# Optimization experiments

Measured on AMD Instinct MI355X. Metric: run time of the kernel, lower is better.

The kernel has to match this reference:

```python
import jax, jax.numpy as jnp
import numpy as np

VOC, TOPIC, EMB, BATCH = 128000, 512, 1024, 1024

def setup_inputs() -> dict:
    key = jax.random.key(0)
    k1, k2, k3 = jax.random.split(key, 3)
    x = jax.random.normal(k1, (TOPIC, BATCH), dtype=jnp.float32)
    beta0 = jax.random.normal(k2, (VOC, EMB), dtype=jnp.float32)
    beta_t = jax.random.normal(k3, (TOPIC, EMB), dtype=jnp.float32) * 0.02  # nn.init.normal_(std=0.02)
    return {"x": x, "beta0": beta0, "beta_t": beta_t, "t": 0}

def reference(x, beta0, beta_t, t):
    # w: [voc, topic] = beta0 [voc, emb] @ beta_t.T [emb, topic]
    # (the t==0 branch and else branch are identical in the source)
    w = jnp.einsum('ve,te->vt', beta0, beta_t)
    w = jax.nn.softmax(w, axis=0)  # softmax over vocab dim (dim=0)
    # out: [voc, batch]
    return jnp.einsum('vt,tb->vb', w, x)
```

## Files before the change

kernel.cpp:

```cpp
#include <hip/hip_runtime.h>

typedef _Float16 f16x8 __attribute__((ext_vector_type(8)));
typedef float    f32x4 __attribute__((ext_vector_type(4)));
typedef unsigned short u16;

#define VOC   128000
#define TOPIC 512
#define EMB   1024
#define BATCH 1024
#define ROWB  128

__device__ __forceinline__ int swz(int row, int kbyte) {
    return row * ROWB + (kbyte ^ ((row & 7) << 4));
}
__device__ __forceinline__ int xcd_swz(int bid, int nwg) {
    int x = bid & 7, o = bid >> 3, q = nwg >> 3, r = nwg & 7;
    return (x < r ? x * (q + 1) : r * (q + 1) + (x - r) * q) + o;
}
union H2U { _Float16 h; u16 u; };

#define SBAR() asm volatile("s_barrier" ::: "memory")
#define WVM0() asm volatile("s_waitcnt vmcnt(0)" ::: "memory")
#define WLG0() asm volatile("s_waitcnt lgkmcnt(0)" ::: "memory")

#define GLDS(SRC, DST) __builtin_amdgcn_global_load_lds( \
    (const __attribute__((address_space(1))) unsigned int*)(SRC), \
    (__attribute__((address_space(3))) unsigned int*)(DST), 16, 0, 0)

#define RD_A(MH, KS) { _Pragma("unroll") \
    for (int m = 0; m < 4; ++m) \
        af[m] = *(const f16x8*)(bufA + wr * 16384 + \
            swz((MH) * 64 + m * 16 + lr, (KS) * 64 + lk * 16)); }
#define RD_B(KS) { _Pragma("unroll") \
    for (int n = 0; n < 4; ++n) \
        bf[n] = *(const f16x8*)(bufB + (wc >> 1) * 16384 + \
            swz((wc & 1) * 64 + n * 16 + lr, (KS) * 64 + lk * 16)); }
#define MFMA16(MH) { \
    __builtin_amdgcn_s_setprio(1); \
    _Pragma("unroll") for (int m = 0; m < 4; ++m) \
    _Pragma("unroll") for (int n = 0; n < 4; ++n) \
        acc[(MH) * 4 + m][n] = __builtin_amdgcn_mfma_f32_16x16x32_f16( \
            af[m], bf[n], acc[(MH) * 4 + m][n], 0, 0, 0); \
    __builtin_amdgcn_s_setprio(0); }

__global__ void cvt_betat_kernel(const float* __restrict__ betat, u16* __restrict__ bt16) {
    const size_t g = (size_t)blockIdx.x * 256 + threadIdx.x;
    const float4* src = reinterpret_cast<const float4*>(betat) + g * 2;
    float4 a = src[0], b = src[1];
    f16x8 h;
    h[0]=(_Float16)a.x; h[1]=(_Float16)a.y; h[2]=(_Float16)a.z; h[3]=(_Float16)a.w;
    h[4]=(_Float16)b.x; h[5]=(_Float16)b.y; h[6]=(_Float16)b.z; h[7]=(_Float16)b.w;
    *(reinterpret_cast<f16x8*>(bt16) + g) = h;
}

__global__ __launch_bounds__(512, 2) void gemm1_kernel(
    const float* __restrict__ beta0, const u16* __restrict__ bt16,
    u16* __restrict__ Eg, float* __restrict__ sg)
{
    __shared__ char lds[131072];

    const int tid  = threadIdx.x;
    const int lane = tid & 63;
    const int wid  = tid >> 6;
    const int wr = wid >> 2, wc = wid & 3;
    const int lr = lane & 15, lk = lane >> 4;
    const int srow8  = lane >> 3;
    const int schunk = ((lane & 7) ^ srow8) * 8;

    const int bid   = xcd_swz(blockIdx.x, gridDim.x);
    const int tile  = bid >> 1;
    const int chunk = bid & 1;
    const int v0 = tile * 256, t0 = chunk * 256;

    const int a_row = tid >> 1, a_kh = tid & 1;
    const float* aRowP = beta0 + (size_t)(v0 + a_row) * EMB + a_kh * 32;

    f32x4 acc[8][4] = {};
    f16x8 af[4], bf[4];
    float4 rA[8];

    auto loadA4 = [&](int kt, int j0) {
        const float4* g = reinterpret_cast<const float4*>(aRowP + kt * 64);
        #pragma unroll
        for (int j = 0; j < 4; ++j) rA[j0 + j] = g[j0 + j];
    };
    auto cvtA = [&](int kt1, int j0) {
        char* dA = lds + (kt1 & 1) * 65536 + (a_row >> 7) * 16384;
        const int rl = a_row & 127;
        #pragma unroll
        for (int jj = 0; jj < 2; ++jj) {
            float4 xx = rA[j0 + jj * 2], yy = rA[j0 + jj * 2 + 1];
            f16x8 h;
            h[0]=(_Float16)xx.x; h[1]=(_Float16)xx.y; h[2]=(_Float16)xx.z; h[3]=(_Float16)xx.w;
            h[4]=(_Float16)yy.x; h[5]=(_Float16)yy.y; h[6]=(_Float16)yy.z; h[7]=(_Float16)yy.w;
            *(f16x8*)(dA + swz(rl, (a_kh * 4 + (j0 >> 1) + jj) * 16)) = h;
        }
    };
    auto stageB = [&](int kt, int h) {
        char* dstb = lds + (kt & 1) * 65536 + 32768 + h * 16384;
        #pragma unroll
        for (int q = 0; q < 2; ++q) {
            const u16* s_ = bt16 + (size_t)(t0 + h * 128 + wid * 16 + q * 8 + srow8) * EMB
                          + kt * 64 + schunk;
            GLDS(s_, dstb + (wid * 16 + q * 8) * ROWB);
        }
    };

    loadA4(0, 0); loadA4(0, 4);
    stageB(0, 0); stageB(0, 1);
    cvtA(0, 0); cvtA(0, 4);
    WLG0();

    for (int t = 0; t < 16; ++t) {
        char* bufA = lds + (t & 1) * 65536;
        char* bufB = bufA + 32768;
        const bool st = (t + 1) < 16;

        WVM0();
        SBAR();
        RD_A(0, 0); RD_B(0);
        if (st) { loadA4(t + 1, 0); stageB(t + 1, 0); }
        MFMA16(0);
        SBAR();
        RD_A(1, 0);
        if (st) { loadA4(t + 1, 4); stageB(t + 1, 1); }
        MFMA16(1);
        SBAR();
        RD_A(0, 1); RD_B(1);
        if (st) cvtA(t + 1, 0);
        MFMA16(0);
        SBAR();
        RD_A(1, 1);
        if (st) cvtA(t + 1, 4);
        MFMA16(1);
        WLG0();
    }

    __syncthreads();
    u16* ldsE = reinterpret_cast<u16*>(lds);
    float csum = 0.f;
    #pragma unroll
    for (int c = 0; c < 4; ++c) {
        if (wr == (c >> 1)) {
            const int mb = (c & 1) * 4;
            #pragma unroll
            for (int m = 0; m < 4; ++m)
              #pragma unroll
              for (int n = 0; n < 4; ++n)
                #pragma unroll
                for (int r = 0; r < 4; ++r) {
                    const int row = m * 16 + lk * 4 + r;
                    const int col = wc * 64 + n * 16 + lr;
                    H2U cv; cv.h = (_Float16)__expf(acc[mb + m][n][r]);
                    ldsE[row * 264 + col] = cv.u;
                }
        }
        __syncthreads();
        {
            const int row8 = tid >> 3, seg = tid & 7;
            const int4* sp = reinterpret_cast<const int4*>(&ldsE[row8 * 264 + seg * 32]);
            u16* dst = Eg + (size_t)(v0 + c * 64 + row8) * 2048 + t0 + seg * 32;
            int4 a0 = sp[0], a1 = sp[1], a2 = sp[2], a3 = sp[3];
            int4* dp = reinterpret_cast<int4*>(dst);
            dp[0] = a0; dp[1] = a1; dp[2] = a2; dp[3] = a3;
        }
        if (tid < 256) {
            float s = 0.f;
            for (int r = 0; r < 64; ++r) { H2U cv; cv.u = ldsE[r * 264 + tid]; s += (float)cv.h; }
            csum += s;
        }
        __syncthreads();
    }
    if (tid < 256) atomicAdd(sg + t0 + tid, csum);
}

__global__ void xst_kernel(const float* __restrict__ x, const float* __restrict__ s,
                           u16* __restrict__ xsT)
{
    __shared__ float tile[32][33];
    const int b0 = blockIdx.x * 32, t0 = blockIdx.y * 32;
    const int tx = threadIdx.x, ty = threadIdx.y;
    tile[ty][tx] = x[(size_t)(t0 + ty) * BATCH + b0 + tx];
    __syncthreads();
    const float sc = 65536.0f / s[t0 + tx];
    H2U cv; cv.h = (_Float16)(tile[tx][ty] * sc);
    xsT[(size_t)(b0 + ty) * TOPIC + t0 + tx] = cv.u;
}

__global__ __launch_bounds__(512, 2) void gemm2_kernel(
    const u16* __restrict__ Eg, const u16* __restrict__ xsT,
    float* __restrict__ out, int c0, int nch)
{
    __shared__ char lds[131072];

    const int tid  = threadIdx.x;
    const int lane = tid & 63;
    const int wid  = tid >> 6;
    const int wr = wid >> 2, wc = wid & 3;
    const int lr = lane & 15, lk = lane >> 4;
    const int srow8  = lane >> 3;
    const int schunk = ((lane & 7) ^ srow8) * 8;

    const int bid   = xcd_swz(blockIdx.x, gridDim.x);
    const int tile  = bid / nch;
    const int chunk = bid % nch;
    const int v0 = tile * 256, b0 = (c0 + chunk) * 256;

    f32x4 acc[8][4] = {};
    f16x8 af[4], bf[4];

    auto stageA = [&](int kt, int h) {
        char* dsta = lds + (kt & 1) * 65536 + h * 16384;
        #pragma unroll
        for (int q = 0; q < 2; ++q) {
            const u16* s_ = Eg + (size_t)(v0 + h * 128 + wid * 16 + q * 8 + srow8) * 2048
                          + kt * 64 + schunk;
            GLDS(s_, dsta + (wid * 16 + q * 8) * ROWB);
        }
    };
    auto stageB = [&](int kt, int h) {
        char* dstb = lds + (kt & 1) * 65536 + 32768 + h * 16384;
        #pragma unroll
        for (int q = 0; q < 2; ++q) {
            const u16* s_ = xsT + (size_t)(b0 + h * 128 + wid * 16 + q * 8 + srow8) * TOPIC
                          + kt * 64 + schunk;
            GLDS(s_, dstb + (wid * 16 + q * 8) * ROWB);
        }
    };

    stageA(0, 0); stageA(0, 1); stageB(0, 0); stageB(0, 1);

    for (int t = 0; t < 8; ++t) {
        char* bufA = lds + (t & 1) * 65536;
        char* bufB = bufA + 32768;
        const bool st = (t + 1) < 8;

        WVM0();
        SBAR();
        RD_A(0, 0); RD_B(0);
        if (st) stageA(t + 1, 0);
        MFMA16(0);
        SBAR();
        RD_A(1, 0);
        if (st) stageA(t + 1, 1);
        MFMA16(1);
        SBAR();
        RD_A(0, 1); RD_B(1);
        if (st) stageB(t + 1, 0);
        MFMA16(0);
        SBAR();
        RD_A(1, 1);
        if (st) stageB(t + 1, 1);
        MFMA16(1);
    }

    #pragma unroll
    for (int mh = 0; mh < 2; ++mh)
      #pragma unroll
      for (int m = 0; m < 4; ++m)
        #pragma unroll
        for (int n = 0; n < 4; ++n)
          #pragma unroll
          for (int r = 0; r < 4; ++r) {
              const int row = wr * 128 + mh * 64 + m * 16 + lk * 4 + r;
              const int col = wc * 64 + n * 16 + lr;
              out[(size_t)(v0 + row) * BATCH + b0 + col] = acc[mh * 4 + m][n][r] * 0x1p-16f;
          }
}

extern "C" void kernel_launch(void* const* d_in, const int* in_sizes, int n_in,
                              void* d_out, int out_size, void* d_ws, size_t ws_size,
                              hipStream_t stream)
{
    const float* x     = (const float*)d_in[0];
    const float* beta0 = (const float*)d_in[1];
    const float* betat = (const float*)d_in[2];
    float* out = (float*)d_out;

    const size_t need_min = 4096 + (size_t)BATCH * TOPIC * 2;
    if (ws_size < need_min) return;
    float* s_g  = (float*)d_ws;
    u16*   buf1 = (u16*)((char*)d_ws + 4096);

    hipMemsetAsync(d_ws, 0, 2048, stream);
    cvt_betat_kernel<<<256, 256, 0, stream>>>(betat, buf1);

    u16* EgO = (u16*)d_out;
    gemm1_kernel<<<1000, 512, 0, stream>>>(beta0, buf1, EgO, s_g);

    xst_kernel<<<dim3(BATCH / 32, TOPIC / 32), dim3(32, 32), 0, stream>>>(x, s_g, buf1);

    gemm2_kernel<<<1500, 512, 0, stream>>>(EgO, buf1, out, 1, 3);
    gemm2_kernel<<<500,  512, 0, stream>>>(EgO, buf1, out, 0, 1);
}
```

Measured before the change: 569.5 us.

## Replace pipelined 256x256 GEMM kernels with simple single-buffered 128-tile versions

Both GEMM kernels drop the double-buffered, hand-scheduled pipeline with raw s_barrier/waitcnt and priority hints. They become simpler single-buffered loops with smaller tiles: 128x128 with 256 threads for gemm1, and 128x256 with 512 threads for gemm2. Launch grids are scaled up to match, and LDS use shrinks so more blocks can share a CU. This trades the intra-block overlap of loads and MFMA for occupancy and more blocks, at the cost of re-reading beta0 four times across topic chunks and exposing load latency at every k-step.

After: 717.2 us. +25.9%, slower.

```diff
diff --git a/kernel.cpp b/kernel.cpp
--- a/kernel.cpp
+++ b/kernel.cpp
@@ -19,29 +19,9 @@
 }
 union H2U { _Float16 h; u16 u; };
 
-#define SBAR() asm volatile("s_barrier" ::: "memory")
-#define WVM0() asm volatile("s_waitcnt vmcnt(0)" ::: "memory")
-#define WLG0() asm volatile("s_waitcnt lgkmcnt(0)" ::: "memory")
-
 #define GLDS(SRC, DST) __builtin_amdgcn_global_load_lds( \
     (const __attribute__((address_space(1))) unsigned int*)(SRC), \
     (__attribute__((address_space(3))) unsigned int*)(DST), 16, 0, 0)
-
-#define RD_A(MH, KS) { _Pragma("unroll") \
-    for (int m = 0; m < 4; ++m) \
-        af[m] = *(const f16x8*)(bufA + wr * 16384 + \
-            swz((MH) * 64 + m * 16 + lr, (KS) * 64 + lk * 16)); }
-#define RD_B(KS) { _Pragma("unroll") \
-    for (int n = 0; n < 4; ++n) \
-        bf[n] = *(const f16x8*)(bufB + (wc >> 1) * 16384 + \
-            swz((wc & 1) * 64 + n * 16 + lr, (KS) * 64 + lk * 16)); }
-#define MFMA16(MH) { \
-    __builtin_amdgcn_s_setprio(1); \
-    _Pragma("unroll") for (int m = 0; m < 4; ++m) \
-    _Pragma("unroll") for (int n = 0; n < 4; ++n) \
-        acc[(MH) * 4 + m][n] = __builtin_amdgcn_mfma_f32_16x16x32_f16( \
-            af[m], bf[n], acc[(MH) * 4 + m][n], 0, 0, 0); \
-    __builtin_amdgcn_s_setprio(0); }
 
 __global__ void cvt_betat_kernel(const float* __restrict__ betat, u16* __restrict__ bt16) {
     const size_t g = (size_t)blockIdx.x * 256 + threadIdx.x;
@@ -53,125 +33,108 @@
     *(reinterpret_cast<f16x8*>(bt16) + g) = h;
 }
 
-__global__ __launch_bounds__(512, 2) void gemm1_kernel(
+__global__ __launch_bounds__(256) void gemm1_kernel(
     const float* __restrict__ beta0, const u16* __restrict__ bt16,
     u16* __restrict__ Eg, float* __restrict__ sg)
 {
-    __shared__ char lds[131072];
+    __shared__ char lds[32768];
 
     const int tid  = threadIdx.x;
     const int lane = tid & 63;
     const int wid  = tid >> 6;
-    const int wr = wid >> 2, wc = wid & 3;
+    const int wr = wid >> 1, wc = wid & 1;
     const int lr = lane & 15, lk = lane >> 4;
     const int srow8  = lane >> 3;
     const int schunk = ((lane & 7) ^ srow8) * 8;
 
-    const int bid   = xcd_swz(blockIdx.x, gridDim.x);
-    const int tile  = bid >> 1;
-    const int chunk = bid & 1;
-    const int v0 = tile * 256, t0 = chunk * 256;
-
-    const int a_row = tid >> 1, a_kh = tid & 1;
-    const float* aRowP = beta0 + (size_t)(v0 + a_row) * EMB + a_kh * 32;
-
-    f32x4 acc[8][4] = {};
-    f16x8 af[4], bf[4];
+    const int bid = xcd_swz(blockIdx.x, gridDim.x);
+    const int t0  = (bid & 3) * 128;
+    const int v0  = (bid >> 2) * 128;
+
+    const int arow = tid >> 1, ahalf = tid & 1;
+    const float* aBase = beta0 + (size_t)(v0 + arow) * EMB + ahalf * 32;
+
     float4 rA[8];
-
-    auto loadA4 = [&](int kt, int j0) {
-        const float4* g = reinterpret_cast<const float4*>(aRowP + kt * 64);
-        #pragma unroll
-        for (int j = 0; j < 4; ++j) rA[j0 + j] = g[j0 + j];
+    f16x8  af[4], bf[4];
+    f32x4  acc[4][4] = {};
+
+    auto loadA = [&](int kt) {
+        const float4* g = reinterpret_cast<const float4*>(aBase + kt * 64);
+        #pragma unroll
+        for (int j = 0; j < 8; ++j) rA[j] = g[j];
     };
-    auto cvtA = [&](int kt1, int j0) {
-        char* dA = lds + (kt1 & 1) * 65536 + (a_row >> 7) * 16384;
-        const int rl = a_row & 127;
-        #pragma unroll
-        for (int jj = 0; jj < 2; ++jj) {
-            float4 xx = rA[j0 + jj * 2], yy = rA[j0 + jj * 2 + 1];
+    auto cvtA = [&]() {
+        #pragma unroll
+        for (int jj = 0; jj < 4; ++jj) {
+            float4 x = rA[jj * 2], y = rA[jj * 2 + 1];
             f16x8 h;
-            h[0]=(_Float16)xx.x; h[1]=(_Float16)xx.y; h[2]=(_Float16)xx.z; h[3]=(_Float16)xx.w;
-            h[4]=(_Float16)yy.x; h[5]=(_Float16)yy.y; h[6]=(_Float16)yy.z; h[7]=(_Float16)yy.w;
-            *(f16x8*)(dA + swz(rl, (a_kh * 4 + (j0 >> 1) + jj) * 16)) = h;
+            h[0]=(_Float16)x.x; h[1]=(_Float16)x.y; h[2]=(_Float16)x.z; h[3]=(_Float16)x.w;
+            h[4]=(_Float16)y.x; h[5]=(_Float16)y.y; h[6]=(_Float16)y.z; h[7]=(_Float16)y.w;
+            *(f16x8*)(lds + swz(arow, (ahalf * 4 + jj) * 16)) = h;
         }
     };
-    auto stageB = [&](int kt, int h) {
-        char* dstb = lds + (kt & 1) * 65536 + 32768 + h * 16384;
-        #pragma unroll
-        for (int q = 0; q < 2; ++q) {
-            const u16* s_ = bt16 + (size_t)(t0 + h * 128 + wid * 16 + q * 8 + srow8) * EMB
-                          + kt * 64 + schunk;
-            GLDS(s_, dstb + (wid * 16 + q * 8) * ROWB);
+    auto stageB = [&](int kt) {
+        #pragma unroll
+        for (int g = 0; g < 4; ++g) {
+            const u16* s = bt16 + (size_t)(t0 + wid * 32 + g * 8 + srow8) * EMB
+                         + kt * 64 + schunk;
+            GLDS(s, lds + 16384 + (wid * 32 + g * 8) * ROWB);
         }
     };
 
-    loadA4(0, 0); loadA4(0, 4);
-    stageB(0, 0); stageB(0, 1);
-    cvtA(0, 0); cvtA(0, 4);
-    WLG0();
-
-    for (int t = 0; t < 16; ++t) {
-        char* bufA = lds + (t & 1) * 65536;
-        char* bufB = bufA + 32768;
-        const bool st = (t + 1) < 16;
-
-        WVM0();
-        SBAR();
-        RD_A(0, 0); RD_B(0);
-        if (st) { loadA4(t + 1, 0); stageB(t + 1, 0); }
-        MFMA16(0);
-        SBAR();
-        RD_A(1, 0);
-        if (st) { loadA4(t + 1, 4); stageB(t + 1, 1); }
-        MFMA16(1);
-        SBAR();
-        RD_A(0, 1); RD_B(1);
-        if (st) cvtA(t + 1, 0);
-        MFMA16(0);
-        SBAR();
-        RD_A(1, 1);
-        if (st) cvtA(t + 1, 4);
-        MFMA16(1);
-        WLG0();
+    loadA(0);
+
+    for (int kt = 0; kt < 16; ++kt) {
+        __syncthreads();
+        stageB(kt);
+        cvtA();
+        __syncthreads();
+        if (kt + 1 < 16) loadA(kt + 1);
+        #pragma unroll
+        for (int ks = 0; ks < 2; ++ks) {
+            #pragma unroll
+            for (int m = 0; m < 4; ++m)
+                af[m] = *(const f16x8*)(lds + swz(wr * 64 + m * 16 + lr, ks * 64 + lk * 16));
+            #pragma unroll
+            for (int n = 0; n < 4; ++n)
+                bf[n] = *(const f16x8*)(lds + 16384 + swz(wc * 64 + n * 16 + lr, ks * 64 + lk * 16));
+            #pragma unroll
+            for (int m = 0; m < 4; ++m)
+                #pragma unroll
+                for (int n = 0; n < 4; ++n)
+                    acc[m][n] = __builtin_amdgcn_mfma_f32_16x16x32_f16(
+                        af[m], bf[n], acc[m][n], 0, 0, 0);
+        }
     }
 
     __syncthreads();
     u16* ldsE = reinterpret_cast<u16*>(lds);
-    float csum = 0.f;
     #pragma unroll
-    for (int c = 0; c < 4; ++c) {
-        if (wr == (c >> 1)) {
-            const int mb = (c & 1) * 4;
-            #pragma unroll
-            for (int m = 0; m < 4; ++m)
-              #pragma unroll
-              for (int n = 0; n < 4; ++n)
-                #pragma unroll
-                for (int r = 0; r < 4; ++r) {
-                    const int row = m * 16 + lk * 4 + r;
-                    const int col = wc * 64 + n * 16 + lr;
-                    H2U cv; cv.h = (_Float16)__expf(acc[mb + m][n][r]);
-                    ldsE[row * 264 + col] = cv.u;
-                }
-        }
-        __syncthreads();
-        {
-            const int row8 = tid >> 3, seg = tid & 7;
-            const int4* sp = reinterpret_cast<const int4*>(&ldsE[row8 * 264 + seg * 32]);
-            u16* dst = Eg + (size_t)(v0 + c * 64 + row8) * 2048 + t0 + seg * 32;
-            int4 a0 = sp[0], a1 = sp[1], a2 = sp[2], a3 = sp[3];
-            int4* dp = reinterpret_cast<int4*>(dst);
-            dp[0] = a0; dp[1] = a1; dp[2] = a2; dp[3] = a3;
-        }
-        if (tid < 256) {
-            float s = 0.f;
-            for (int r = 0; r < 64; ++r) { H2U cv; cv.u = ldsE[r * 264 + tid]; s += (float)cv.h; }
-            csum += s;
-        }
-        __syncthreads();
-    }
-    if (tid < 256) atomicAdd(sg + t0 + tid, csum);
+    for (int m = 0; m < 4; ++m)
+      #pragma unroll
+      for (int n = 0; n < 4; ++n)
+        #pragma unroll
+        for (int r = 0; r < 4; ++r) {
+            const int row = wr * 64 + m * 16 + lk * 4 + r;
+            const int col = wc * 64 + n * 16 + lr;
+            H2U cv; cv.h = (_Float16)__expf(acc[m][n][r]);
+            ldsE[row * 128 + col] = cv.u;
+        }
+    __syncthreads();
+    {
+        const int row = tid >> 1, half = tid & 1;
+        u16* dst = Eg + (size_t)(v0 + row) * 2048 + t0 + half * 64;
+        #pragma unroll
+        for (int i = 0; i < 8; ++i) {
+            int4 vv = *reinterpret_cast<const int4*>(&ldsE[row * 128 + half * 64 + i * 8]);
+            *reinterpret_cast<int4*>(dst + i * 8) = vv;
+        }
+    }
+    if (tid < 128) {
+        float sum = 0.f;
+        for (int r = 0; r < 128; ++r) { H2U cv; cv.u = ldsE[r * 128 + tid]; sum += (float)cv.h; }
+        atomicAdd(sg + t0 + tid, sum);
+    }
 }
 
 __global__ void xst_kernel(const float* __restrict__ x, const float* __restrict__ s,
@@ -187,11 +150,11 @@
     xsT[(size_t)(b0 + ty) * TOPIC + t0 + tx] = cv.u;
 }
 
-__global__ __launch_bounds__(512, 2) void gemm2_kernel(
+__global__ __launch_bounds__(512) void gemm2_kernel(
     const u16* __restrict__ Eg, const u16* __restrict__ xsT,
     float* __restrict__ out, int c0, int nch)
 {
-    __shared__ char lds[131072];
+    __shared__ char lds[49152];
 
     const int tid  = threadIdx.x;
     const int lane = tid & 63;
@@ -204,68 +167,53 @@
     const int bid   = xcd_swz(blockIdx.x, gridDim.x);
     const int tile  = bid / nch;
     const int chunk = bid % nch;
-    const int v0 = tile * 256, b0 = (c0 + chunk) * 256;
-
-    f32x4 acc[8][4] = {};
+    const int v0 = tile * 128, b0 = (c0 + chunk) * 256;
+
     f16x8 af[4], bf[4];
-
-    auto stageA = [&](int kt, int h) {
-        char* dsta = lds + (kt & 1) * 65536 + h * 16384;
-        #pragma unroll
-        for (int q = 0; q < 2; ++q) {
-            const u16* s_ = Eg + (size_t)(v0 + h * 128 + wid * 16 + q * 8 + srow8) * 2048
-                          + kt * 64 + schunk;
-            GLDS(s_, dsta + (wid * 16 + q * 8) * ROWB);
-        }
-    };
-    auto stageB = [&](int kt, int h) {
-        char* dstb = lds + (kt & 1) * 65536 + 32768 + h * 16384;
-        #pragma unroll
-        for (int q = 0; q < 2; ++q) {
-            const u16* s_ = xsT + (size_t)(b0 + h * 128 + wid * 16 + q * 8 + srow8) * TOPIC
-                          + kt * 64 + schunk;
-            GLDS(s_, dstb + (wid * 16 + q * 8) * ROWB);
-        }
-    };
-
-    stageA(0, 0); stageA(0, 1); stageB(0, 0); stageB(0, 1);
-
-    for (int t = 0; t < 8; ++t) {
-        char* bufA = lds + (t & 1) * 65536;
-        char* bufB = bufA + 32768;
-        const bool st = (t + 1) < 8;
-
-        WVM0();
-        SBAR();
-        RD_A(0, 0); RD_B(0);
-        if (st) stageA(t + 1, 0);
-        MFMA16(0);
-        SBAR();
-        RD_A(1, 0);
-        if (st) stageA(t + 1, 1);
-        MFMA16(1);
-        SBAR();
-        RD_A(0, 1); RD_B(1);
-        if (st) stageB(t + 1, 0);
-        MFMA16(0);
-        SBAR();
-        RD_A(1, 1);
-        if (st) stageB(t + 1, 1);
-        MFMA16(1);
+    f32x4 acc[4][4] = {};
+
+    for (int kt = 0; kt < 8; ++kt) {
+        __syncthreads();
+        #pragma unroll
+        for (int g = 0; g < 2; ++g) {
+            const u16* s = Eg + (size_t)(v0 + wid * 16 + g * 8 + srow8) * 2048
+                         + kt * 64 + schunk;
+            GLDS(s, lds + (wid * 16 + g * 8) * ROWB);
+        }
+        #pragma unroll
+        for (int g = 0; g < 4; ++g) {
+            const u16* s = xsT + (size_t)(b0 + wid * 32 + g * 8 + srow8) * TOPIC
+                         + kt * 64 + schunk;
+            GLDS(s, lds + 16384 + (wid * 32 + g * 8) * ROWB);
+        }
+        __syncthreads();
+        #pragma unroll
+        for (int ks = 0; ks < 2; ++ks) {
+            #pragma unroll
+            for (int m = 0; m < 4; ++m)
+                af[m] = *(const f16x8*)(lds + swz(wr * 64 + m * 16 + lr, ks * 64 + lk * 16));
+            #pragma unroll
+            for (int n = 0; n < 4; ++n)
+                bf[n] = *(const f16x8*)(lds + 16384 + swz(wc * 64 + n * 16 + lr, ks * 64 + lk * 16));
+            #pragma unroll
+            for (int m = 0; m < 4; ++m)
+                #pragma unroll
+                for (int n = 0; n < 4; ++n)
+                    acc[m][n] = __builtin_amdgcn_mfma_f32_16x16x32_f16(
+                        af[m], bf[n], acc[m][n], 0, 0, 0);
+        }
     }
 
     #pragma unroll
-    for (int mh = 0; mh < 2; ++mh)
+    for (int m = 0; m < 4; ++m)
       #pragma unroll
-      for (int m = 0; m < 4; ++m)
-        #pragma unroll
-        for (int n = 0; n < 4; ++n)
-          #pragma unroll
-          for (int r = 0; r < 4; ++r) {
-              const int row = wr * 128 + mh * 64 + m * 16 + lk * 4 + r;
-              const int col = wc * 64 + n * 16 + lr;
-              out[(size_t)(v0 + row) * BATCH + b0 + col] = acc[mh * 4 + m][n][r] * 0x1p-16f;
-          }
+      for (int n = 0; n < 4; ++n)
+        #pragma unroll
+        for (int r = 0; r < 4; ++r) {
+            const int row = wr * 64 + m * 16 + lk * 4 + r;
+            const int col = wc * 64 + n * 16 + lr;
+            out[(size_t)(v0 + row) * BATCH + b0 + col] = acc[m][n][r] * 0x1p-16f;
+        }
 }
 
 extern "C" void kernel_launch(void* const* d_in, const int* in_sizes, int n_in,
@@ -286,10 +234,10 @@
     cvt_betat_kernel<<<256, 256, 0, stream>>>(betat, buf1);
 
     u16* EgO = (u16*)d_out;
-    gemm1_kernel<<<1000, 512, 0, stream>>>(beta0, buf1, EgO, s_g);
+    gemm1_kernel<<<4000, 256, 0, stream>>>(beta0, buf1, EgO, s_g);
 
     xst_kernel<<<dim3(BATCH / 32, TOPIC / 32), dim3(32, 32), 0, stream>>>(x, s_g, buf1);
 
-    gemm2_kernel<<<1500, 512, 0, stream>>>(EgO, buf1, out, 1, 3);
-    gemm2_kernel<<<500,  512, 0, stream>>>(EgO, buf1, out, 0, 1);
-}
+    gemm2_kernel<<<3000, 512, 0, stream>>>(EgO, buf1, out, 1, 3);
+    gemm2_kernel<<<1000, 512, 0, stream>>>(EgO, buf1, out, 0, 1);
+}
```
